# Kernel optimization log

Measured on AMD Instinct MI355X. Metric: run time of the kernel, lower is better.

Reference implementation:

```python
import jax, jax.numpy as jnp
import numpy as np

# ---- static config (matches init_kwargs / input_specs) ----
MODEL_CONTEXT_LEN = 4096
BLOCK_SIZE = 16
NUM_Q_HEADS = 32
NUM_KV_HEADS = 8
HEAD_DIM = 128
ROPE_BASE = 10000.0
B = 8
NUM_PAST = 4613                                   # context_len - 1, same for all seqs
END_BNUM = NUM_PAST // BLOCK_SIZE                 # 288
REM = NUM_PAST % BLOCK_SIZE                       # 5
START_BNUM = (NUM_PAST - MODEL_CONTEXT_LEN) // BLOCK_SIZE + 2  # 34
CUR_POS = MODEL_CONTEXT_LEN - 1                   # 4095 (capped decode position)
BLOCKS_PER_SEQ = END_BNUM + 1                     # 289
NUM_BLOCKS = B * BLOCKS_PER_SEQ                   # 2312


def rope(pos, x):
    """NeoX-style rotary. pos: [T] int; x: [..., T, H, D]."""
    half = HEAD_DIM // 2
    inv = 1.0 / (ROPE_BASE ** (jnp.arange(half, dtype=jnp.float32) / half))
    freqs = pos.astype(jnp.float32)[:, None] * inv        # [T, half]
    cos = jnp.cos(freqs)[:, None, :]                      # [T, 1, half]
    sin = jnp.sin(freqs)[:, None, :]
    x1, x2 = jnp.split(x, 2, axis=-1)
    return jnp.concatenate([x1 * cos - x2 * sin, x2 * cos + x1 * sin], axis=-1)


def setup_inputs() -> dict:
    key = jax.random.key(0)
    ks = jax.random.split(key, 7)
    q = jax.random.normal(ks[0], (B, NUM_Q_HEADS * HEAD_DIM), jnp.float32)
    k = jax.random.normal(ks[1], (B, NUM_KV_HEADS * HEAD_DIM), jnp.float32)
    v = jax.random.normal(ks[2], (B, NUM_KV_HEADS * HEAD_DIM), jnp.float32)
    positions = jnp.full((B,), NUM_PAST, dtype=jnp.int32)
    context_lens = jnp.full((B,), NUM_PAST + 1, dtype=jnp.int32)
    # distinct physical blocks per sequence (paged layout)
    block_tables = jnp.arange(NUM_BLOCKS, dtype=jnp.int32).reshape(B, BLOCKS_PER_SEQ)
    # cache stores UN-rotated keys (module writes k_original); layout [nblk, bs, Hk, D]
    key_cache = jax.random.normal(ks[3], (NUM_BLOCKS, BLOCK_SIZE, NUM_KV_HEADS, HEAD_DIM), jnp.float32) * 0.5
    value_cache = jax.random.normal(ks[4], (NUM_BLOCKS, BLOCK_SIZE, NUM_KV_HEADS, HEAD_DIM), jnp.float32) * 0.5
    W_o = jax.random.normal(ks[5], (NUM_Q_HEADS * HEAD_DIM, NUM_Q_HEADS * HEAD_DIM), jnp.float32) * 0.02
    return {"q": q, "k": k, "v": v, "positions": positions, "context_lens": context_lens,
            "block_tables": block_tables, "key_cache": key_cache, "value_cache": value_cache, "W_o": W_o}


def reference(q, k, v, positions, context_lens, block_tables, key_cache, value_cache, W_o):
    # Decode path of StreamingAttentionSink, context > model_context_len:
    # gather sink block + sliding-window blocks, re-apply rotary at shifted
    # positions, attend with q/k roped at capped position, project output.
    # positions for re-roped past keys: sink tokens 0..bs-1, window tokens
    # 2*bs-1-rem .. model_context_len-2 (matches the torch code's pos arange).
    pos_sink = np.arange(BLOCK_SIZE)
    pos_win = np.arange(2 * BLOCK_SIZE - 1 - REM, MODEL_CONTEXT_LEN - 1)
    POS = jnp.asarray(np.concatenate([pos_sink, pos_win]), dtype=jnp.int32)  # [4085]

    qh = q.reshape(B, NUM_Q_HEADS, HEAD_DIM)
    kh = k.reshape(B, NUM_KV_HEADS, HEAD_DIM)
    vh = v.reshape(B, NUM_KV_HEADS, HEAD_DIM)

    # phys_bnums = [block_table[0]] + block_table[start:end]  -> [B, 255]
    phys = jnp.concatenate([block_tables[:, :1], block_tables[:, START_BNUM:END_BNUM]], axis=1)
    full_k = key_cache[phys].reshape(B, -1, NUM_KV_HEADS, HEAD_DIM)       # [B, 4080, Hk, D]
    rem_k = key_cache[block_tables[:, END_BNUM], :REM]                     # [B, 5, Hk, D]
    past_k = jnp.concatenate([full_k, rem_k], axis=1)                      # [B, 4085, Hk, D]
    full_v = value_cache[phys].reshape(B, -1, NUM_KV_HEADS, HEAD_DIM)
    rem_v = value_cache[block_tables[:, END_BNUM], :REM]
    past_v = jnp.concatenate([full_v, rem_v], axis=1)

    past_k = rope(POS, past_k)  # re-apply rotary to shifted sink/window keys

    cur = jnp.array([CUR_POS], dtype=jnp.int32)
    q_rot = rope(cur, qh[:, None, :, :])[:, 0]   # [B, H, D] at capped position
    k_rot = rope(cur, kh[:, None, :, :])[:, 0]   # [B, Hk, D]

    keys = jnp.concatenate([past_k, k_rot[:, None]], axis=1)   # [B, 4086, Hk, D]
    vals = jnp.concatenate([past_v, vh[:, None]], axis=1)

    # GQA attention (group = 4 q-heads per kv-head)
    G = NUM_Q_HEADS // NUM_KV_HEADS
    qg = q_rot.reshape(B, NUM_KV_HEADS, G, HEAD_DIM)
    scale = 1.0 / np.sqrt(HEAD_DIM).astype(np.float32)
    scores = jnp.einsum('bhgd,bthd->bhgt', qg, keys) * scale
    probs = jax.nn.softmax(scores, axis=-1)
    attn = jnp.einsum('bhgt,bthd->bhgd', probs, vals).reshape(B, NUM_Q_HEADS * HEAD_DIM)
    return attn @ W_o
```

## Files before the change

### kernel.cpp

```cpp
#include <hip/hip_runtime.h>
#include <math.h>

#define NB 8
#define NQH 32
#define NKVH 8
#define HD 128
#define GQ 4
#define T_TOT 4086
#define SPLITS 16
#define TCHUNK 256
#define TILE 32
#define PAD 132
#define BPS 289
#define LOG2_10K_OVER_64 0.2076205059304601f
#define SCALE 0.08838834764831843f

#define TAB_OFF       0
#define TAB_SZ        (4096 * 128)
#define PART_GEMM_OFF 0
#define PART_ATTN_OFF TAB_SZ
#define PART_ATTN_SZ  (64 * GQ * SPLITS * PAD)
#define ATTN_OFF      (PART_ATTN_OFF + PART_ATTN_SZ)

__global__ __launch_bounds__(256) void rope_table_kernel(float* __restrict__ tab)
{
    int idx = blockIdx.x * 256 + threadIdx.x;
    int pos = idx >> 6, j = idx & 63;
    float inv = exp2f(-(float)j * LOG2_10K_OVER_64);
    float freq = (float)pos * inv;
    float sn, cs; sincosf(freq, &sn, &cs);
    tab[pos * 128 + j]      = cs;
    tab[pos * 128 + 64 + j] = sn;
}

__global__ __launch_bounds__(256) void attn_partial_kernel(
    const float* __restrict__ q, const float* __restrict__ k, const float* __restrict__ v,
    const int* __restrict__ bt, const float* __restrict__ kc, const float* __restrict__ vc,
    const float* __restrict__ tab, float* __restrict__ part)
{
    __shared__ float kt[TILE][PAD];
    __shared__ float vt[TILE][PAD];
    __shared__ float qs[GQ][HD];
    __shared__ float sc[GQ][TILE];

    const int tid  = threadIdx.x;
    const int bh   = blockIdx.x;
    const int s    = blockIdx.y;
    const int b    = bh >> 3, h = bh & 7;
    const int lane = tid & 63, wave = tid >> 6;

    const float* qp = q + (size_t)b * (NQH * HD) + (size_t)h * (GQ * HD);
    const float* trow = tab + 4095 * 128;
    for (int e = tid; e < GQ * HD; e += 256) {
        int g = e >> 7, d = e & 127, j = d & 63;
        float cs = trow[j], sn = trow[64 + j];
        float x1 = qp[g * HD + j], x2 = qp[g * HD + j + 64];
        qs[g][d] = (d < 64) ? (x1 * cs - x2 * sn) : (x2 * cs + x1 * sn);
    }

    float m_run = -INFINITY, l_run = 0.0f, acc_lo = 0.0f, acc_hi = 0.0f;
    const int t0 = s * TCHUNK;
    const int* btb = bt + b * BPS;

    for (int tb = 0; tb < TCHUNK; tb += TILE) {
        __syncthreads();

        for (int e = tid; e < TILE * 16; e += 256) {
            int row = e >> 4, c4 = (e & 15) << 2;
            int tg = t0 + tb + row;
            if (tg <= T_TOT - 1) {
                const float* ksrc; int pos;
                if (tg == T_TOT - 1) {
                    ksrc = k + (size_t)(b * NKVH + h) * HD;
                    pos = 4095;
                } else {
                    int bti, rr;
                    if (tg < 16)        { bti = 0;              rr = tg;        pos = tg;      }
                    else if (tg < 4080) { bti = 33 + (tg >> 4); rr = tg & 15;   pos = tg + 10; }
                    else                { bti = 288;            rr = tg - 4080; pos = tg + 10; }
                    int blk = btb[bti];
                    ksrc = kc + (((size_t)blk * 16 + rr) * NKVH + h) * HD;
                }
                float4 k1 = *(const float4*)(ksrc + c4);
                float4 k2 = *(const float4*)(ksrc + 64 + c4);
                float4 cs = *(const float4*)(tab + (size_t)pos * 128 + c4);
                float4 sn = *(const float4*)(tab + (size_t)pos * 128 + 64 + c4);
                float4 lo, hi;
                lo.x = k1.x * cs.x - k2.x * sn.x;  hi.x = k2.x * cs.x + k1.x * sn.x;
                lo.y = k1.y * cs.y - k2.y * sn.y;  hi.y = k2.y * cs.y + k1.y * sn.y;
                lo.z = k1.z * cs.z - k2.z * sn.z;  hi.z = k2.z * cs.z + k1.z * sn.z;
                lo.w = k1.w * cs.w - k2.w * sn.w;  hi.w = k2.w * cs.w + k1.w * sn.w;
                *(float4*)&kt[row][c4]      = lo;
                *(float4*)&kt[row][64 + c4] = hi;
            } else {
                float4 z = {0.f, 0.f, 0.f, 0.f};
                *(float4*)&kt[row][c4]      = z;
                *(float4*)&kt[row][64 + c4] = z;
            }
        }
        for (int e = tid; e < TILE * 32; e += 256) {
            int row = e >> 5, c4 = (e & 31) << 2;
            int tg = t0 + tb + row;
            if (tg <= T_TOT - 1) {
                const float* vsrc;
                if (tg == T_TOT - 1) {
                    vsrc = v + (size_t)(b * NKVH + h) * HD;
                } else {
                    int bti, rr;
                    if (tg < 16)        { bti = 0;              rr = tg;        }
                    else if (tg < 4080) { bti = 33 + (tg >> 4); rr = tg & 15;   }
                    else                { bti = 288;            rr = tg - 4080; }
                    int blk = btb[bti];
                    vsrc = vc + (((size_t)blk * 16 + rr) * NKVH + h) * HD;
                }
                *(float4*)&vt[row][c4] = *(const float4*)(vsrc + c4);
            } else {
                float4 z = {0.f, 0.f, 0.f, 0.f};
                *(float4*)&vt[row][c4] = z;
            }
        }
        __syncthreads();

        if (tid < 128) {
            int t = tid & 31, g = tid >> 5;
            int tg = t0 + tb + t;
            float dot = 0.f;
            #pragma unroll
            for (int d4 = 0; d4 < 32; ++d4) {
                float4 kk = *(const float4*)&kt[t][d4 << 2];
                float4 qq = *(const float4*)&qs[g][d4 << 2];
                dot += kk.x * qq.x + kk.y * qq.y + kk.z * qq.z + kk.w * qq.w;
            }
            sc[g][t] = (tg <= T_TOT - 1) ? dot * SCALE : -INFINITY;
        }
        __syncthreads();

        {
            int g = wave;
            int tl = lane & 31;
            float sv = sc[g][tl];
            float mx = sv;
            #pragma unroll
            for (int off = 16; off; off >>= 1) mx = fmaxf(mx, __shfl_xor(mx, off));
            float m_new = fmaxf(m_run, mx);
            float alpha = expf(m_run - m_new);
            float p = expf(sv - m_new);
            float ps = p;
            #pragma unroll
            for (int off = 16; off; off >>= 1) ps += __shfl_xor(ps, off);
            l_run = l_run * alpha + ps;
            m_run = m_new;
            acc_lo *= alpha; acc_hi *= alpha;
            if (lane < 32) sc[g][tl] = p;
            #pragma unroll 8
            for (int t = 0; t < TILE; ++t) {
                float pv = sc[g][t];
                acc_lo += pv * vt[t][lane];
                acc_hi += pv * vt[t][lane + 64];
            }
        }
    }

    float* pp = part + ((size_t)(bh * GQ + wave) * SPLITS + s) * PAD;
    pp[lane] = acc_lo;
    pp[lane + 64] = acc_hi;
    if (lane == 0) { pp[128] = m_run; pp[129] = l_run; }
}

__global__ __launch_bounds__(256) void attn_reduce_kernel(
    const float* __restrict__ part, float* __restrict__ attn)
{
    int bh = blockIdx.x;
    int tid = threadIdx.x;
    int g = tid >> 6, lane = tid & 63;
    const float* pg = part + (size_t)(bh * GQ + g) * SPLITS * PAD;
    float mstar = -INFINITY;
    #pragma unroll
    for (int s = 0; s < SPLITS; ++s) mstar = fmaxf(mstar, pg[s * PAD + 128]);
    float accl = 0.f, acch = 0.f, l = 0.f;
    #pragma unroll
    for (int s = 0; s < SPLITS; ++s) {
        float w = expf(pg[s * PAD + 128] - mstar);
        l    += pg[s * PAD + 129] * w;
        accl += w * pg[s * PAD + lane];
        acch += w * pg[s * PAD + lane + 64];
    }
    int b = bh >> 3, h = bh & 7;
    float inv_l = 1.0f / l;
    size_t base = (size_t)b * 4096 + (size_t)(h * GQ + g) * 128;
    attn[base + lane]      = accl * inv_l;
    attn[base + lane + 64] = acch * inv_l;
}

__global__ __launch_bounds__(256) void gemm_partial_kernel(
    const float* __restrict__ attn, const float* __restrict__ Wo,
    float* __restrict__ part)
{
    __shared__ float a_s[NB][256];
    __shared__ float red[4][NB][64];
    int tid = threadIdx.x;
    int lane = tid & 63, w = tid >> 6;
    int jt = blockIdx.x;
    int is = blockIdx.y;
    int i0 = is * 256;
    int c  = jt * 64 + lane;
    for (int e = tid; e < NB * 256; e += 256) {
        int bb = e >> 8, i = e & 255;
        a_s[bb][i] = attn[(size_t)bb * 4096 + i0 + i];
    }
    __syncthreads();
    float acc[NB] = {0.f, 0.f, 0.f, 0.f, 0.f, 0.f, 0.f, 0.f};
    const float* wp = Wo + (size_t)(i0 + w * 64) * 4096 + c;
    #pragma unroll 4
    for (int ii = 0; ii < 64; ++ii) {
        float wv = wp[(size_t)ii * 4096];
        int i_loc = w * 64 + ii;
        #pragma unroll
        for (int bb = 0; bb < NB; ++bb) acc[bb] += a_s[bb][i_loc] * wv;
    }
    #pragma unroll
    for (int bb = 0; bb < NB; ++bb) red[w][bb][lane] = acc[bb];
    __syncthreads();
    for (int e = tid; e < NB * 64; e += 256) {
        int bb = e >> 6, l = e & 63;
        float sum = red[0][bb][l] + red[1][bb][l] + red[2][bb][l] + red[3][bb][l];
        part[(size_t)is * 32768 + (size_t)bb * 4096 + jt * 64 + l] = sum;
    }
}

__global__ __launch_bounds__(256) void gemm_reduce_kernel(
    const float* __restrict__ part, float* __restrict__ out)
{
    int idx = blockIdx.x * 256 + threadIdx.x;
    float4 sum = {0.f, 0.f, 0.f, 0.f};
    #pragma unroll
    for (int s = 0; s < 16; ++s) {
        float4 p = *(const float4*)(part + (size_t)s * 32768 + (size_t)idx * 4);
        sum.x += p.x; sum.y += p.y; sum.z += p.z; sum.w += p.w;
    }
    *(float4*)(out + (size_t)idx * 4) = sum;
}

extern "C" void kernel_launch(void* const* d_in, const int* in_sizes, int n_in,
                              void* d_out, int out_size, void* d_ws, size_t ws_size,
                              hipStream_t stream) {
    const float* q  = (const float*)d_in[0];
    const float* k  = (const float*)d_in[1];
    const float* v  = (const float*)d_in[2];
    const int*   bt = (const int*)d_in[5];
    const float* kc = (const float*)d_in[6];
    const float* vc = (const float*)d_in[7];
    const float* Wo = (const float*)d_in[8];
    float* out = (float*)d_out;
    float* ws  = (float*)d_ws;

    float* tab       = ws + TAB_OFF;
    float* part_attn = ws + PART_ATTN_OFF;
    float* attn      = ws + ATTN_OFF;
    float* part_gemm = ws + PART_GEMM_OFF;

    rope_table_kernel<<<1024, 256, 0, stream>>>(tab);
    attn_partial_kernel<<<dim3(64, SPLITS), 256, 0, stream>>>(q, k, v, bt, kc, vc, tab, part_attn);
    attn_reduce_kernel<<<64, 256, 0, stream>>>(part_attn, attn);
    gemm_partial_kernel<<<dim3(64, 16), 256, 0, stream>>>(attn, Wo, part_gemm);
    gemm_reduce_kernel<<<32, 256, 0, stream>>>(part_gemm, out);
}
```

Before: 380.9 us.

## Prefetch KV tiles into registers, parallelize scores over all waves, widen GEMM columns

The attention kernel now loads the next K/V tile into registers while computing on the current one, so global loads overlap compute. The score computation is spread across all 256 threads, with each half-wave doing half the dot product and combining via a shuffle, which removes a __syncthreads. The P·V loop reads probabilities as float4. The output GEMM has each thread compute two adjacent columns with float2 loads over half as many blocks. The trade-off is higher register pressure from the prefetch buffers and fewer GEMM blocks.

```diff
diff --git a/kernel.cpp b/kernel.cpp
--- a/kernel.cpp
+++ b/kernel.cpp
@@ -33,13 +33,32 @@
     tab[pos * 128 + 64 + j] = sn;
 }
 
+__device__ __forceinline__ void kv_src(int tg, int b, int h, const int* btb,
+                                       const float* k, const float* v,
+                                       const float* kc, const float* vc,
+                                       const float** ks, const float** vs, int* pos)
+{
+    if (tg == T_TOT - 1) {
+        *ks = k + (size_t)(b * NKVH + h) * HD;
+        *vs = v + (size_t)(b * NKVH + h) * HD;
+        *pos = 4095;
+    } else {
+        int bti, rr;
+        if (tg < 16)        { bti = 0;              rr = tg;        *pos = tg;      }
+        else if (tg < 4080) { bti = 33 + (tg >> 4); rr = tg & 15;   *pos = tg + 10; }
+        else                { bti = 288;            rr = tg - 4080; *pos = tg + 10; }
+        size_t off = (((size_t)btb[bti] * 16 + rr) * NKVH + h) * HD;
+        *ks = kc + off; *vs = vc + off;
+    }
+}
+
 __global__ __launch_bounds__(256) void attn_partial_kernel(
     const float* __restrict__ q, const float* __restrict__ k, const float* __restrict__ v,
     const int* __restrict__ bt, const float* __restrict__ kc, const float* __restrict__ vc,
     const float* __restrict__ tab, float* __restrict__ part)
 {
     __shared__ float kt[TILE][PAD];
-    __shared__ float vt[TILE][PAD];
+    __shared__ float vt[TILE][128];
     __shared__ float qs[GQ][HD];
     __shared__ float sc[GQ][TILE];
 
@@ -58,110 +77,116 @@
         qs[g][d] = (d < 64) ? (x1 * cs - x2 * sn) : (x2 * cs + x1 * sn);
     }
 
-    float m_run = -INFINITY, l_run = 0.0f, acc_lo = 0.0f, acc_hi = 0.0f;
     const int t0 = s * TCHUNK;
     const int* btb = bt + b * BPS;
 
+    float4 pk1[2], pk2[2], pcs[2], psn[2], pvv[4];
+    const int kc4 = (tid & 15) << 2;
+    const int vc4 = (tid & 31) << 2;
+
+    auto load_tile = [&](int tb) {
+        #pragma unroll
+        for (int it = 0; it < 2; ++it) {
+            int row = (tid + it * 256) >> 4;
+            int tg = t0 + tb + row;
+            if (tg <= T_TOT - 1) {
+                const float *ks, *vs; int pos;
+                kv_src(tg, b, h, btb, k, v, kc, vc, &ks, &vs, &pos);
+                pk1[it] = *(const float4*)(ks + kc4);
+                pk2[it] = *(const float4*)(ks + 64 + kc4);
+                pcs[it] = *(const float4*)(tab + (size_t)pos * 128 + kc4);
+                psn[it] = *(const float4*)(tab + (size_t)pos * 128 + 64 + kc4);
+            } else {
+                float4 z = {0.f,0.f,0.f,0.f};
+                pk1[it] = z; pk2[it] = z; pcs[it] = z; psn[it] = z;
+            }
+        }
+        #pragma unroll
+        for (int it = 0; it < 4; ++it) {
+            int row = (tid + it * 256) >> 5;
+            int tg = t0 + tb + row;
+            if (tg <= T_TOT - 1) {
+                const float *ks, *vs; int pos;
+                kv_src(tg, b, h, btb, k, v, kc, vc, &ks, &vs, &pos);
+                pvv[it] = *(const float4*)(vs + vc4);
+            } else {
+                float4 z = {0.f,0.f,0.f,0.f};
+                pvv[it] = z;
+            }
+        }
+    };
+
+    auto store_tile = [&]() {
+        #pragma unroll
+        for (int it = 0; it < 2; ++it) {
+            int row = (tid + it * 256) >> 4;
+            float4 k1 = pk1[it], k2 = pk2[it], cs = pcs[it], sn = psn[it];
+            float4 lo, hi;
+            lo.x = k1.x * cs.x - k2.x * sn.x;  hi.x = k2.x * cs.x + k1.x * sn.x;
+            lo.y = k1.y * cs.y - k2.y * sn.y;  hi.y = k2.y * cs.y + k1.y * sn.y;
+            lo.z = k1.z * cs.z - k2.z * sn.z;  hi.z = k2.z * cs.z + k1.z * sn.z;
+            lo.w = k1.w * cs.w - k2.w * sn.w;  hi.w = k2.w * cs.w + k1.w * sn.w;
+            *(float4*)&kt[row][kc4]      = lo;
+            *(float4*)&kt[row][64 + kc4] = hi;
+        }
+        #pragma unroll
+        for (int it = 0; it < 4; ++it) {
+            int row = (tid + it * 256) >> 5;
+            *(float4*)&vt[row][vc4] = pvv[it];
+        }
+    };
+
+    float m_run = -INFINITY, l_run = 0.0f, acc_lo = 0.0f, acc_hi = 0.0f;
+    const int g = wave, tl = lane & 31, half = lane >> 5;
+
+    load_tile(0);
     for (int tb = 0; tb < TCHUNK; tb += TILE) {
         __syncthreads();
-
-        for (int e = tid; e < TILE * 16; e += 256) {
-            int row = e >> 4, c4 = (e & 15) << 2;
-            int tg = t0 + tb + row;
-            if (tg <= T_TOT - 1) {
-                const float* ksrc; int pos;
-                if (tg == T_TOT - 1) {
-                    ksrc = k + (size_t)(b * NKVH + h) * HD;
-                    pos = 4095;
-                } else {
-                    int bti, rr;
-                    if (tg < 16)        { bti = 0;              rr = tg;        pos = tg;      }
-                    else if (tg < 4080) { bti = 33 + (tg >> 4); rr = tg & 15;   pos = tg + 10; }
-                    else                { bti = 288;            rr = tg - 4080; pos = tg + 10; }
-                    int blk = btb[bti];
-                    ksrc = kc + (((size_t)blk * 16 + rr) * NKVH + h) * HD;
-                }
-                float4 k1 = *(const float4*)(ksrc + c4);
-                float4 k2 = *(const float4*)(ksrc + 64 + c4);
-                float4 cs = *(const float4*)(tab + (size_t)pos * 128 + c4);
-                float4 sn = *(const float4*)(tab + (size_t)pos * 128 + 64 + c4);
-                float4 lo, hi;
-                lo.x = k1.x * cs.x - k2.x * sn.x;  hi.x = k2.x * cs.x + k1.x * sn.x;
-                lo.y = k1.y * cs.y - k2.y * sn.y;  hi.y = k2.y * cs.y + k1.y * sn.y;
-                lo.z = k1.z * cs.z - k2.z * sn.z;  hi.z = k2.z * cs.z + k1.z * sn.z;
-                lo.w = k1.w * cs.w - k2.w * sn.w;  hi.w = k2.w * cs.w + k1.w * sn.w;
-                *(float4*)&kt[row][c4]      = lo;
-                *(float4*)&kt[row][64 + c4] = hi;
-            } else {
-                float4 z = {0.f, 0.f, 0.f, 0.f};
-                *(float4*)&kt[row][c4]      = z;
-                *(float4*)&kt[row][64 + c4] = z;
-            }
-        }
-        for (int e = tid; e < TILE * 32; e += 256) {
-            int row = e >> 5, c4 = (e & 31) << 2;
-            int tg = t0 + tb + row;
-            if (tg <= T_TOT - 1) {
-                const float* vsrc;
-                if (tg == T_TOT - 1) {
-                    vsrc = v + (size_t)(b * NKVH + h) * HD;
-                } else {
-                    int bti, rr;
-                    if (tg < 16)        { bti = 0;              rr = tg;        }
-                    else if (tg < 4080) { bti = 33 + (tg >> 4); rr = tg & 15;   }
-                    else                { bti = 288;            rr = tg - 4080; }
-                    int blk = btb[bti];
-                    vsrc = vc + (((size_t)blk * 16 + rr) * NKVH + h) * HD;
-                }
-                *(float4*)&vt[row][c4] = *(const float4*)(vsrc + c4);
-            } else {
-                float4 z = {0.f, 0.f, 0.f, 0.f};
-                *(float4*)&vt[row][c4] = z;
-            }
-        }
+        store_tile();
         __syncthreads();
-
-        if (tid < 128) {
-            int t = tid & 31, g = tid >> 5;
-            int tg = t0 + tb + t;
-            float dot = 0.f;
+        if (tb + TILE < TCHUNK) load_tile(tb + TILE);
+
+        float dot = 0.f;
+        {
+            const float* kr = &kt[tl][half * 64];
+            const float* qr = &qs[g][half * 64];
             #pragma unroll
-            for (int d4 = 0; d4 < 32; ++d4) {
-                float4 kk = *(const float4*)&kt[t][d4 << 2];
-                float4 qq = *(const float4*)&qs[g][d4 << 2];
+            for (int j4 = 0; j4 < 16; ++j4) {
+                float4 kk = *(const float4*)(kr + (j4 << 2));
+                float4 qq = *(const float4*)(qr + (j4 << 2));
                 dot += kk.x * qq.x + kk.y * qq.y + kk.z * qq.z + kk.w * qq.w;
             }
-            sc[g][t] = (tg <= T_TOT - 1) ? dot * SCALE : -INFINITY;
-        }
-        __syncthreads();
-
-        {
-            int g = wave;
-            int tl = lane & 31;
-            float sv = sc[g][tl];
-            float mx = sv;
-            #pragma unroll
-            for (int off = 16; off; off >>= 1) mx = fmaxf(mx, __shfl_xor(mx, off));
-            float m_new = fmaxf(m_run, mx);
-            float alpha = expf(m_run - m_new);
-            float p = expf(sv - m_new);
-            float ps = p;
-            #pragma unroll
-            for (int off = 16; off; off >>= 1) ps += __shfl_xor(ps, off);
-            l_run = l_run * alpha + ps;
-            m_run = m_new;
-            acc_lo *= alpha; acc_hi *= alpha;
-            if (lane < 32) sc[g][tl] = p;
-            #pragma unroll 8
-            for (int t = 0; t < TILE; ++t) {
-                float pv = sc[g][t];
-                acc_lo += pv * vt[t][lane];
-                acc_hi += pv * vt[t][lane + 64];
-            }
-        }
-    }
-
-    float* pp = part + ((size_t)(bh * GQ + wave) * SPLITS + s) * PAD;
+        }
+        dot += __shfl_xor(dot, 32);
+        int tg = t0 + tb + tl;
+        float sv = (tg <= T_TOT - 1) ? dot * SCALE : -INFINITY;
+
+        float mx = sv;
+        #pragma unroll
+        for (int off = 16; off; off >>= 1) mx = fmaxf(mx, __shfl_xor(mx, off));
+        float m_new = fmaxf(m_run, mx);
+        float alpha = expf(m_run - m_new);
+        float p = expf(sv - m_new);
+        float ps = p;
+        #pragma unroll
+        for (int off = 16; off; off >>= 1) ps += __shfl_xor(ps, off);
+        l_run = l_run * alpha + ps;
+        m_run = m_new;
+        acc_lo *= alpha; acc_hi *= alpha;
+        if (lane < 32) sc[g][tl] = p;
+
+        #pragma unroll
+        for (int t4 = 0; t4 < 8; ++t4) {
+            float4 p4 = *(const float4*)&sc[g][t4 << 2];
+            int t = t4 << 2;
+            acc_lo += p4.x * vt[t][lane]     + p4.y * vt[t+1][lane]
+                    + p4.z * vt[t+2][lane]   + p4.w * vt[t+3][lane];
+            acc_hi += p4.x * vt[t][lane+64]  + p4.y * vt[t+1][lane+64]
+                    + p4.z * vt[t+2][lane+64]+ p4.w * vt[t+3][lane+64];
+        }
+    }
+
+    float* pp = part + ((size_t)(bh * GQ + g) * SPLITS + s) * PAD;
     pp[lane] = acc_lo;
     pp[lane + 64] = acc_hi;
     if (lane == 0) { pp[128] = m_run; pp[129] = l_run; }
@@ -197,34 +222,41 @@
     float* __restrict__ part)
 {
     __shared__ float a_s[NB][256];
-    __shared__ float red[4][NB][64];
+    __shared__ float red[4][NB][128];
     int tid = threadIdx.x;
     int lane = tid & 63, w = tid >> 6;
     int jt = blockIdx.x;
     int is = blockIdx.y;
     int i0 = is * 256;
-    int c  = jt * 64 + lane;
+    int c  = jt * 128 + lane * 2;
     for (int e = tid; e < NB * 256; e += 256) {
         int bb = e >> 8, i = e & 255;
         a_s[bb][i] = attn[(size_t)bb * 4096 + i0 + i];
     }
     __syncthreads();
-    float acc[NB] = {0.f, 0.f, 0.f, 0.f, 0.f, 0.f, 0.f, 0.f};
+    float accx[NB] = {}, accy[NB] = {};
     const float* wp = Wo + (size_t)(i0 + w * 64) * 4096 + c;
-    #pragma unroll 4
+    #pragma unroll 8
     for (int ii = 0; ii < 64; ++ii) {
-        float wv = wp[(size_t)ii * 4096];
-        int i_loc = w * 64 + ii;
-        #pragma unroll
-        for (int bb = 0; bb < NB; ++bb) acc[bb] += a_s[bb][i_loc] * wv;
-    }
-    #pragma unroll
-    for (int bb = 0; bb < NB; ++bb) red[w][bb][lane] = acc[bb];
+        float2 wv = *(const float2*)(wp + (size_t)ii * 4096);
+        int il = w * 64 + ii;
+        #pragma unroll
+        for (int bb = 0; bb < NB; ++bb) {
+            float a = a_s[bb][il];
+            accx[bb] += a * wv.x;
+            accy[bb] += a * wv.y;
+        }
+    }
+    #pragma unroll
+    for (int bb = 0; bb < NB; ++bb) {
+        red[w][bb][lane * 2]     = accx[bb];
+        red[w][bb][lane * 2 + 1] = accy[bb];
+    }
     __syncthreads();
-    for (int e = tid; e < NB * 64; e += 256) {
-        int bb = e >> 6, l = e & 63;
+    for (int e = tid; e < NB * 128; e += 256) {
+        int bb = e >> 7, l = e & 127;
         float sum = red[0][bb][l] + red[1][bb][l] + red[2][bb][l] + red[3][bb][l];
-        part[(size_t)is * 32768 + (size_t)bb * 4096 + jt * 64 + l] = sum;
+        part[(size_t)is * 32768 + (size_t)bb * 4096 + jt * 128 + l] = sum;
     }
 }
 
@@ -262,6 +294,6 @@
     rope_table_kernel<<<1024, 256, 0, stream>>>(tab);
     attn_partial_kernel<<<dim3(64, SPLITS), 256, 0, stream>>>(q, k, v, bt, kc, vc, tab, part_attn);
     attn_reduce_kernel<<<64, 256, 0, stream>>>(part_attn, attn);
-    gemm_partial_kernel<<<dim3(64, 16), 256, 0, stream>>>(attn, Wo, part_gemm);
+    gemm_partial_kernel<<<dim3(32, 16), 256, 0, stream>>>(attn, Wo, part_gemm);
     gemm_reduce_kernel<<<32, 256, 0, stream>>>(part_gemm, out);
 }
```

After: 384.7 us. No clear change (+1.0%).
